# Performance work log

Hardware: AMD Instinct MI355X
Metric: run time of the kernel (lower is better)

Reference implementation:

```python
import jax, jax.numpy as jnp
import numpy as np

N_BATCH, D_FEAT, N_CLASSES = 96, 64, 21
MARGIN = 0.3


def setup_inputs() -> dict:
    key = jax.random.key(0)
    k1, k2, k3 = jax.random.split(key, 3)
    logits = jax.random.normal(k1, (N_BATCH, D_FEAT), dtype=jnp.float32)
    feat2 = jax.random.normal(k2, (N_BATCH, D_FEAT), dtype=jnp.float32)
    labels = (jax.random.uniform(k3, (N_BATCH, N_CLASSES)) < 0.3).astype(jnp.float32)
    return {"logits": logits, "labels": labels, "feat2": feat2}


def reference(logits, labels, feat2):
    """Dense-mask formulation of QuadrupletMarginMiner (defaults:
    margin=0.3, type_of_quadruplets='all', what_is_hard='one').

    Instead of a data-dependent list of quadruplets, returns a boolean
    tensor valid[i, j, k, n] that is True exactly for the quadruplets the
    torch module would return (same set, dense encoding).
    """
    n = labels.shape[0]
    eps = 1e-12

    # --- label structure ------------------------------------------------
    s = (labels @ labels.T) > 0                      # share-a-label matrix
    diffs = ~s                                       # torch: sames ^ 1 (pre diag fill)
    sames = s & ~jnp.eye(n, dtype=bool)              # fill_diagonal_(0)
    jk_triu = jnp.triu(jnp.ones((n, n), dtype=bool), k=1)  # strict j < k

    # valid (I, J, K) triples: AP1 & AP2 & j<k   -> [n, n, n]
    triple = sames[:, :, None] & sames[:, None, :] & jk_triu[None, :, :]
    # attach every negative N: diffs[i, n]        -> [n, n, n, n]
    quad = triple[:, :, :, None] & diffs[:, None, None, :]

    # --- distances (negative cosine similarity) ---------------------------
    xn = logits / jnp.maximum(jnp.linalg.norm(logits, axis=1, keepdims=True), eps)
    yn = feat2 / jnp.maximum(jnp.linalg.norm(feat2, axis=1, keepdims=True), eps)
    mat = -(xn @ yn.T)                               # [n, n]

    # margin_p[i, p, neg] = mat[i, neg] - mat[i, p]  (p stands for J or K)
    margin_pn = mat[:, None, :] - mat[:, :, None]    # [i, p, neg]
    viol = margin_pn <= MARGIN                       # [i, p, neg] bool

    # 'all' quadruplets + 'one' hardness: (margin1 <= m) | (margin2 <= m)
    cond = viol[:, :, None, :] | viol[:, None, :, :]  # [i, j, k, neg]

    return quad & cond
```

## Files before the change

### kernel.cpp

```cpp
#include <hip/hip_runtime.h>
#include <math.h>

#define NB 96
#define NB2 (NB * NB)
#define DFEAT 64
#define NCLS 21
#define MARGIN 0.3

typedef int i4 __attribute__((ext_vector_type(4)));

__global__ void precompute_kernel(const float* __restrict__ logits,
                                  const float* __restrict__ labels,
                                  const float* __restrict__ feat2,
                                  double* __restrict__ mat,
                                  double* __restrict__ thr,
                                  unsigned char* __restrict__ share) {
    int gid = blockIdx.x * blockDim.x + threadIdx.x;
    if (gid >= NB2) return;
    int i = gid / NB;
    int j = gid - i * NB;

    const float* xi = logits + i * DFEAT;
    const float* yj = feat2 + j * DFEAT;
    double nx = 0.0, ny = 0.0, dot = 0.0;
#pragma unroll
    for (int d = 0; d < DFEAT; ++d) {
        double a = (double)xi[d];
        double b = (double)yj[d];
        nx += a * a;
        ny += b * b;
        dot += a * b;
    }
    nx = fmax(sqrt(nx), 1e-12);
    ny = fmax(sqrt(ny), 1e-12);
    double m = -(dot / (nx * ny));
    mat[gid] = m;
    thr[gid] = MARGIN + m;

    const float* li = labels + i * NCLS;
    const float* lj = labels + j * NCLS;
    float ldot = 0.f;
#pragma unroll
    for (int c = 0; c < NCLS; ++c) ldot += li[c] * lj[c];
    share[gid] = (ldot > 0.f) ? 1 : 0;
}

__global__ __launch_bounds__(256) void quad_kernel(const double* __restrict__ mat,
                                                   const double* __restrict__ thr,
                                                   const unsigned char* __restrict__ share,
                                                   int* __restrict__ out) {
    const int bid = blockIdx.x;
    const int i = bid / NB;
    const int j = bid - i * NB;
    const int tid = threadIdx.x;

    __shared__ double smat[NB];
    __shared__ double sthr[NB];
    __shared__ unsigned char svalid[NB];

    if (tid < NB) {
        unsigned char s = share[i * NB + tid];
        double m = mat[i * NB + tid];
        smat[tid] = s ? 1e300 : m;
        sthr[tid] = thr[i * NB + tid];
        svalid[tid] = (s && tid != i) ? 1 : 0;
    }
    __syncthreads();

    const bool sames_ij = (svalid[j] != 0);
    const double thr_ij = sthr[j];
    i4* outp = (i4*)(out + (size_t)bid * (size_t)(NB * NB));

#pragma unroll
    for (int r = 0; r < 9; ++r) {
        int c = r * 256 + tid;
        int k = c / 24;
        int q = c - k * 24;
        i4 v = (i4)(0);
        if (sames_ij && svalid[k] && (j < k)) {
            double t = fmax(thr_ij, sthr[k]);
            int n0 = q * 4;
            v.x = (smat[n0 + 0] <= t) ? 1 : 0;
            v.y = (smat[n0 + 1] <= t) ? 1 : 0;
            v.z = (smat[n0 + 2] <= t) ? 1 : 0;
            v.w = (smat[n0 + 3] <= t) ? 1 : 0;
        }
        __builtin_nontemporal_store(v, &outp[c]);
    }
}

extern "C" void kernel_launch(void* const* d_in, const int* in_sizes, int n_in,
                              void* d_out, int out_size, void* d_ws, size_t ws_size,
                              hipStream_t stream) {
    const float* logits = (const float*)d_in[0];
    const float* labels = (const float*)d_in[1];
    const float* feat2  = (const float*)d_in[2];
    int* out = (int*)d_out;

    double* mat = (double*)d_ws;
    double* thr = mat + NB2;
    unsigned char* share = (unsigned char*)(thr + NB2);

    precompute_kernel<<<(NB2 + 255) / 256, 256, 0, stream>>>(logits, labels, feat2,
                                                             mat, thr, share);
    quad_kernel<<<NB2, 256, 0, stream>>>(mat, thr, share, out);
}
```

Before: 342.5 us.

## Precompute per-(i,p) violation bitmasks and select by max threshold

Adds a mask kernel that packs, for each (i,p), a 96-bit mask of negatives n with diffs[i,n] and mat[i,n] <= MARGIN+mat[i,p]. The quad kernel then picks whichever of j or k has the larger threshold and expands that bitmask into the output, so the per-element double compares drop out. The main kernel is bound by output stores, so the saved compute may not matter much, and the extra launch adds overhead.

```diff
diff --git a/kernel.cpp b/kernel.cpp
--- a/kernel.cpp
+++ b/kernel.cpp
@@ -8,6 +8,7 @@
 #define MARGIN 0.3
 
 typedef int i4 __attribute__((ext_vector_type(4)));
+typedef unsigned int u32;
 
 __global__ void precompute_kernel(const float* __restrict__ logits,
                                   const float* __restrict__ labels,
@@ -45,46 +46,72 @@
     share[gid] = (ldot > 0.f) ? 1 : 0;
 }
 
-__global__ __launch_bounds__(256) void quad_kernel(const double* __restrict__ mat,
-                                                   const double* __restrict__ thr,
+__global__ void mask_kernel(const double* __restrict__ mat,
+                            const double* __restrict__ thr,
+                            const unsigned char* __restrict__ share,
+                            u32* __restrict__ mask4) {
+    int gid = blockIdx.x * blockDim.x + threadIdx.x;
+    if (gid >= NB2) return;
+    int i = gid / NB;
+    double t = thr[gid];
+    const double* mrow = mat + i * NB;
+    const unsigned char* srow = share + i * NB;
+    u32 w0 = 0, w1 = 0, w2 = 0;
+#pragma unroll
+    for (int n = 0; n < 32; ++n)
+        if (!srow[n] && (mrow[n] <= t)) w0 |= (1u << n);
+#pragma unroll
+    for (int n = 0; n < 32; ++n)
+        if (!srow[32 + n] && (mrow[32 + n] <= t)) w1 |= (1u << n);
+#pragma unroll
+    for (int n = 0; n < 32; ++n)
+        if (!srow[64 + n] && (mrow[64 + n] <= t)) w2 |= (1u << n);
+    mask4[gid * 4 + 0] = w0;
+    mask4[gid * 4 + 1] = w1;
+    mask4[gid * 4 + 2] = w2;
+    mask4[gid * 4 + 3] = 0;
+}
+
+__global__ __launch_bounds__(256) void quad_kernel(const double* __restrict__ thr,
                                                    const unsigned char* __restrict__ share,
+                                                   const u32* __restrict__ mask4,
                                                    int* __restrict__ out) {
     const int bid = blockIdx.x;
     const int i = bid / NB;
     const int j = bid - i * NB;
     const int tid = threadIdx.x;
 
-    __shared__ double smat[NB];
-    __shared__ double sthr[NB];
-    __shared__ unsigned char svalid[NB];
+    __shared__ u32 vrow[NB][4];
 
     if (tid < NB) {
-        unsigned char s = share[i * NB + tid];
-        double m = mat[i * NB + tid];
-        smat[tid] = s ? 1e300 : m;
-        sthr[tid] = thr[i * NB + tid];
-        svalid[tid] = (s && tid != i) ? 1 : 0;
+        const int k = tid;
+        const double thr_j = thr[i * NB + j];
+        const bool sames_ij = share[i * NB + j] && (j != i);
+        const bool ok = sames_ij && share[i * NB + k] && (k != i) && (j < k);
+        u32 r0 = 0, r1 = 0, r2 = 0;
+        if (ok) {
+            int p = (thr[i * NB + k] > thr_j) ? k : j;
+            const u32* mp = mask4 + (size_t)(i * NB + p) * 4;
+            r0 = mp[0]; r1 = mp[1]; r2 = mp[2];
+        }
+        vrow[k][0] = r0; vrow[k][1] = r1; vrow[k][2] = r2; vrow[k][3] = 0;
     }
     __syncthreads();
 
-    const bool sames_ij = (svalid[j] != 0);
-    const double thr_ij = sthr[j];
-    i4* outp = (i4*)(out + (size_t)bid * (size_t)(NB * NB));
+    i4* outp = (i4*)(out + (size_t)bid * (size_t)NB2);
 
 #pragma unroll
     for (int r = 0; r < 9; ++r) {
         int c = r * 256 + tid;
         int k = c / 24;
         int q = c - k * 24;
-        i4 v = (i4)(0);
-        if (sames_ij && svalid[k] && (j < k)) {
-            double t = fmax(thr_ij, sthr[k]);
-            int n0 = q * 4;
-            v.x = (smat[n0 + 0] <= t) ? 1 : 0;
-            v.y = (smat[n0 + 1] <= t) ? 1 : 0;
-            v.z = (smat[n0 + 2] <= t) ? 1 : 0;
-            v.w = (smat[n0 + 3] <= t) ? 1 : 0;
-        }
+        u32 w = vrow[k][q >> 3];
+        u32 b = w >> ((q & 7) * 4);
+        i4 v;
+        v.x = (int)(b & 1u);
+        v.y = (int)((b >> 1) & 1u);
+        v.z = (int)((b >> 2) & 1u);
+        v.w = (int)((b >> 3) & 1u);
         __builtin_nontemporal_store(v, &outp[c]);
     }
 }
@@ -100,8 +127,12 @@
     double* mat = (double*)d_ws;
     double* thr = mat + NB2;
     unsigned char* share = (unsigned char*)(thr + NB2);
+    size_t off = (size_t)(share + NB2 - (unsigned char*)d_ws);
+    off = (off + 15) & ~(size_t)15;
+    u32* mask4 = (u32*)((unsigned char*)d_ws + off);
 
     precompute_kernel<<<(NB2 + 255) / 256, 256, 0, stream>>>(logits, labels, feat2,
                                                              mat, thr, share);
-    quad_kernel<<<NB2, 256, 0, stream>>>(mat, thr, share, out);
+    mask_kernel<<<(NB2 + 255) / 256, 256, 0, stream>>>(mat, thr, share, mask4);
+    quad_kernel<<<NB2, 256, 0, stream>>>(thr, share, mask4, out);
 }
```

Measured after the change: 357.9 us. +4.5%, slower.
